# Optimization experiments

Measured on AMD Instinct MI355X. Metric: run time of the kernel, lower is better.

## Reference

```python
import jax, jax.numpy as jnp
import numpy as np

N_NODES = 100000
N_EDGES = 3200000
IN_DIM = 128
HID_DIM = 64
OUT_DIM = 2
N_GRAPHS = 512


def setup_inputs() -> dict:
    key = jax.random.key(0)
    ks = jax.random.split(key, 8)
    x = jax.random.normal(ks[0], (N_NODES, IN_DIM), dtype=jnp.float32)
    edge_index = jax.random.randint(ks[1], (2, N_EDGES), 0, N_NODES, dtype=jnp.int64)
    batch = jnp.sort(jax.random.randint(ks[2], (N_NODES,), 0, N_GRAPHS, dtype=jnp.int64))
    # GCNConv params (glorot-ish scale)
    W_gcn = jax.random.normal(ks[3], (IN_DIM, HID_DIM), dtype=jnp.float32) / np.sqrt(IN_DIM)
    b_gcn = jnp.zeros((HID_DIM,), dtype=jnp.float32)
    # MLP params: Linear(hid,hid) -> ReLU -> Linear(hid,out)
    W1 = jax.random.normal(ks[4], (HID_DIM, HID_DIM), dtype=jnp.float32) / np.sqrt(HID_DIM)
    b1 = jnp.zeros((HID_DIM,), dtype=jnp.float32)
    W2 = jax.random.normal(ks[5], (HID_DIM, OUT_DIM), dtype=jnp.float32) / np.sqrt(HID_DIM)
    b2 = jnp.zeros((OUT_DIM,), dtype=jnp.float32)
    return {"x": x, "edge_index": edge_index, "batch": batch,
            "W_gcn": W_gcn, "b_gcn": b_gcn, "W1": W1, "b1": b1, "W2": W2, "b2": b2}


def reference(x, edge_index, batch, W_gcn, b_gcn, W1, b1, W2, b2):
    n = x.shape[0]
    # --- GCNConv: add self-loops, symmetric normalization, aggregate, transform ---
    self_loop = jnp.arange(n, dtype=edge_index.dtype)
    row = jnp.concatenate([edge_index[0], self_loop])  # source nodes
    col = jnp.concatenate([edge_index[1], self_loop])  # target nodes
    deg = jax.ops.segment_sum(jnp.ones_like(col, dtype=x.dtype), col, num_segments=n)
    dinv = jnp.where(deg > 0, jax.lax.rsqrt(deg), 0.0)
    norm = dinv[row] * dinv[col]                       # (E+N,)
    xw = x @ W_gcn                                     # (N, hid) transform first (in_dim > hid)
    msg = xw[row] * norm[:, None]                      # gather + scale
    z = jax.ops.segment_sum(msg, col, num_segments=n) + b_gcn  # scatter-add
    z = jax.nn.relu(z)
    # --- global mean pool over graphs ---
    sums = jax.ops.segment_sum(z, batch, num_segments=N_GRAPHS)          # (G, hid)
    cnts = jax.ops.segment_sum(jnp.ones((n,), z.dtype), batch, num_segments=N_GRAPHS)
    g = sums / jnp.maximum(cnts, 1.0)[:, None]
    # --- MLP -> sigmoid ---
    h = jax.nn.relu(g @ W1 + b1)
    return jax.nn.sigmoid(h @ W2 + b2)                 # (G, out_dim)
```

## Files before the change

### kernel.cpp

```cpp
#include <hip/hip_runtime.h>

#define N_NODES 100000
#define N_EDGES 3200000
#define IN_DIM 128
#define HID_DIM 64
#define OUT_DIM 2
#define N_GRAPHS 512

#define BSHIFT 6
#define NBUCK 1564
#define NB3 256
#define EPB 12500
#define NSB 391
#define LDS_E2 2816
#define ZERO_ROW N_NODES

__device__ inline int xcol(int b) { return ((b & 7) << 5) | (b >> 3); }

__device__ inline float uaf(unsigned int u) {
    union { unsigned int i; float f; } v; v.i = u; return v.f;
}
__device__ inline unsigned short f2bf(float f) {
    union { float f; unsigned int i; } v; v.f = f;
    unsigned int r = v.i + 0x7fffu + ((v.i >> 16) & 1u);
    return (unsigned short)(r >> 16);
}

typedef __attribute__((ext_vector_type(8))) short bf16x8;
typedef __attribute__((ext_vector_type(4))) float f32x4;
typedef __attribute__((ext_vector_type(2))) float f32x2;

__global__ __launch_bounds__(512) void k_hist(const int* __restrict__ col,
                                              int* __restrict__ H) {
    __shared__ int h[NBUCK];
    for (int i = threadIdx.x; i < NBUCK; i += 512) h[i] = 0;
    __syncthreads();
    int b = blockIdx.x;
    int bb = xcol(b);
    int s = b * EPB, e = s + EPB;
    for (int i = s + threadIdx.x; i < e; i += 512)
        atomicAdd(&h[col[i] >> BSHIFT], 1);
    __syncthreads();
    for (int i = threadIdx.x; i < NBUCK; i += 512)
        H[i * NB3 + bb] = h[i];
}

__global__ __launch_bounds__(1024) void k_scan_a(const int* __restrict__ H,
                                                 int* __restrict__ OFF,
                                                 int* __restrict__ bsum) {
    __shared__ int lds[1024];
    int i = blockIdx.x * 1024 + threadIdx.x;
    int v = H[i];
    lds[threadIdx.x] = v;
    __syncthreads();
    for (int off = 1; off < 1024; off <<= 1) {
        int t = (threadIdx.x >= off) ? lds[threadIdx.x - off] : 0;
        __syncthreads();
        lds[threadIdx.x] += t;
        __syncthreads();
    }
    OFF[i] = lds[threadIdx.x] - v;
    if (threadIdx.x == 1023) bsum[blockIdx.x] = lds[1023];
}

__global__ __launch_bounds__(1024) void k_scan_b(int* __restrict__ OFF,
                                                 const int* __restrict__ bsum,
                                                 float* __restrict__ gsum,
                                                 float* __restrict__ gcnt,
                                                 unsigned char* __restrict__ xws) {
    __shared__ int ls[NSB];
    for (int i = threadIdx.x; i < NSB; i += 1024) ls[i] = bsum[i];
    __syncthreads();
    if (threadIdx.x == 0) {
        int run = 0;
        for (int b = 0; b < NSB; b++) { int t = ls[b]; ls[b] = run; run += t; }
    }
    __syncthreads();
    int i = blockIdx.x * 1024 + threadIdx.x;
    OFF[i] += ls[blockIdx.x];
    if (blockIdx.x < 32) gsum[blockIdx.x * 1024 + threadIdx.x] = 0.f;
    if (blockIdx.x == 33 && threadIdx.x < N_GRAPHS) gcnt[threadIdx.x] = 0.f;
    if (blockIdx.x == 32 && threadIdx.x < 16)
        ((int*)(xws + (size_t)ZERO_ROW * HID_DIM))[threadIdx.x] = 0;
}

__global__ __launch_bounds__(512) void k_scatter(const int* __restrict__ row,
                                                 const int* __restrict__ col,
                                                 const int* __restrict__ OFF,
                                                 int* __restrict__ binned) {
    __shared__ int lofs[NBUCK];
    __shared__ int cur[NBUCK];
    int b = blockIdx.x;
    int bb = xcol(b);
    for (int i = threadIdx.x; i < NBUCK; i += 512) {
        lofs[i] = OFF[i * NB3 + bb];
        cur[i] = 0;
    }
    __syncthreads();
    int s = b * EPB, e = s + EPB;
    for (int i = s + threadIdx.x; i < e; i += 512) {
        int c = col[i];
        int r = row[i];
        int bk = c >> BSHIFT;
        int rk = atomicAdd(&cur[bk], 1);
        binned[lofs[bk] + rk] = ((c & 63) << 17) | r;
    }
}

__global__ __launch_bounds__(256) void k_deg(const int* __restrict__ binned,
                                             const int* __restrict__ OFF,
                                             int* __restrict__ degs,
                                             float* __restrict__ dinv) {
    int bkt = blockIdx.x;
    int s = OFF[bkt * NB3];
    int e = (bkt == NBUCK - 1) ? N_EDGES : OFF[(bkt + 1) * NB3];
    __shared__ int cnt[64];
    if (threadIdx.x < 64) cnt[threadIdx.x] = 0;
    __syncthreads();
    for (int i = s + threadIdx.x; i < e; i += 256)
        atomicAdd(&cnt[binned[i] >> 17], 1);
    __syncthreads();
    int n = (bkt << BSHIFT) + threadIdx.x;
    if (threadIdx.x < 64 && n < N_NODES) {
        degs[n] = cnt[threadIdx.x];
        dinv[n] = rsqrtf((float)cnt[threadIdx.x] + 1.0f);
    }
}

__global__ __launch_bounds__(256) void k_gemm(const float* __restrict__ x,
                                              const float* __restrict__ Wg,
                                              const float* __restrict__ dinv,
                                              unsigned char* __restrict__ xws) {
    __shared__ unsigned short wb[16][64][8];

    for (int idx = threadIdx.x; idx < 1024; idx += 256) {
        int f = idx >> 6, l = idx & 63;
        int ks = f >> 2, nt = f & 3;
        int n = (l & 15) + (nt << 4);
        int kbase = (ks << 5) + ((l >> 4) << 3);
        unsigned short tmp[8];
#pragma unroll
        for (int j = 0; j < 8; j++)
            tmp[j] = f2bf(Wg[(kbase + j) * HID_DIM + n]);
        *(bf16x8*)&wb[f][l][0] = *(const bf16x8*)tmp;
    }
    __syncthreads();

    int wave = threadIdx.x >> 6;
    int lane = threadIdx.x & 63;
    int q = lane >> 4, nn = lane & 15;

    bf16x8 bfrag[4][4];
#pragma unroll
    for (int ks = 0; ks < 4; ks++)
#pragma unroll
        for (int nt = 0; nt < 4; nt++)
            bfrag[ks][nt] = *(const bf16x8*)&wb[ks * 4 + nt][lane][0];

    int node0 = blockIdx.x * 64 + wave * 16;
    int arow = node0 + nn;
    if (arow > N_NODES - 1) arow = N_NODES - 1;
    const float* xrow = x + (size_t)arow * IN_DIM + (q << 3);

    f32x4 acc[4] = {{0.f,0.f,0.f,0.f},{0.f,0.f,0.f,0.f},
                    {0.f,0.f,0.f,0.f},{0.f,0.f,0.f,0.f}};
#pragma unroll
    for (int ks = 0; ks < 4; ks++) {
        float4 xa = *(const float4*)(xrow + ks * 32);
        float4 xb_ = *(const float4*)(xrow + ks * 32 + 4);
        bf16x8 af;
        af[0] = (short)f2bf(xa.x); af[1] = (short)f2bf(xa.y);
        af[2] = (short)f2bf(xa.z); af[3] = (short)f2bf(xa.w);
        af[4] = (short)f2bf(xb_.x); af[5] = (short)f2bf(xb_.y);
        af[6] = (short)f2bf(xb_.z); af[7] = (short)f2bf(xb_.w);
#pragma unroll
        for (int nt = 0; nt < 4; nt++)
            acc[nt] = __builtin_amdgcn_mfma_f32_16x16x32_bf16(af, bfrag[ks][nt], acc[nt], 0, 0, 0);
    }

#pragma unroll
    for (int r = 0; r < 4; r++) {
        int mrow = node0 + q * 4 + r;
        if (mrow < N_NODES) {
            float dn = dinv[mrow];
            int p01 = __builtin_amdgcn_cvt_pk_fp8_f32(acc[0][r] * dn, acc[1][r] * dn, 0, false);
            int p23 = __builtin_amdgcn_cvt_pk_fp8_f32(acc[2][r] * dn, acc[3][r] * dn, 0, false);
            unsigned char* rp = xws + (size_t)mrow * HID_DIM + nn;
            rp[0]  = (unsigned char)(p01 & 0xff);
            rp[16] = (unsigned char)((p01 >> 8) & 0xff);
            rp[32] = (unsigned char)(p23 & 0xff);
            rp[48] = (unsigned char)((p23 >> 8) & 0xff);
        }
    }
}

__global__ __launch_bounds__(512) void k_aggrf(const unsigned char* __restrict__ xws,
                                               const int* __restrict__ binned,
                                               const int* __restrict__ OFF,
                                               const int* __restrict__ degs,
                                               const int* __restrict__ batch,
                                               const float* __restrict__ bg,
                                               float* __restrict__ gsum,
                                               float* __restrict__ gcnt) {
    int bkt = blockIdx.x;
    int nbase = bkt << BSHIFT;
    if (nbase >= N_NODES) return;
    int nnodes = N_NODES - nbase; if (nnodes > 64) nnodes = 64;
    int s = OFF[bkt * NB3];
    int e = (bkt == NBUCK - 1) ? N_EDGES : OFF[(bkt + 1) * NB3];
    int m = e - s;

    __shared__ int cnt[64];
    __shared__ int lptr[65];
    __shared__ int cur[64];
    __shared__ int sb[64];
    __shared__ float gcl[8];
    __shared__ alignas(16) int srt[LDS_E2];
    __shared__ float pool[8][4][64];

    if (threadIdx.x < 64) {
        int n = nbase + threadIdx.x;
        cnt[threadIdx.x] = (threadIdx.x < nnodes) ? degs[n] : 0;
        sb[threadIdx.x]  = (threadIdx.x < nnodes) ? batch[n] : 0;
        cur[threadIdx.x] = 0;
    }
    if (threadIdx.x < 8) gcl[threadIdx.x] = 0.f;
    for (int t = threadIdx.x; t < 8 * 4 * 64; t += 512)
        ((float*)pool)[t] = 0.f;
    __syncthreads();

    if (threadIdx.x < 64) {
        int v = (threadIdx.x < nnodes) ? ((cnt[threadIdx.x] + 8) & ~7) : 0;
        int run = v;
#pragma unroll
        for (int off = 1; off < 64; off <<= 1) {
            int t = __shfl_up(run, off);
            if (threadIdx.x >= off) run += t;
        }
        lptr[threadIdx.x + 1] = run;
        if (threadIdx.x == 0) lptr[0] = 0;
    }
    __syncthreads();
    int tot = lptr[64]; if (tot > LDS_E2) tot = LDS_E2;
    for (int i = threadIdx.x; i < tot; i += 512) srt[i] = ZERO_ROW << 6;
    __syncthreads();
    if (threadIdx.x < nnodes) {
        int p = lptr[threadIdx.x] + cnt[threadIdx.x];
        if (p < LDS_E2) srt[p] = (nbase + threadIdx.x) << 6;
        int sl = sb[threadIdx.x] - sb[0];
        if (sl < 8) atomicAdd(&gcl[sl], 1.0f);
        else atomicAdd(&gcnt[sb[threadIdx.x]], 1.0f);
    }
    for (int i = threadIdx.x; i < m; i += 512) {
        int pk = binned[s + i];
        int nid = pk >> 17;
        int rk = atomicAdd(&cur[nid], 1);
        int pos = lptr[nid] + rk;
        if (pos < LDS_E2) srt[pos] = (pk & 0x1FFFF) << 6;
    }
    __syncthreads();

    int wave = threadIdx.x >> 6;
    int lane = threadIdx.x & 63;
    int sub = lane >> 4;
    int lc  = lane & 15;
    int l4  = lc << 2;
    const unsigned char* xbl = xws + l4;
    int g0 = sb[0];
    float4 bia = ((const float4*)bg)[lc];

#pragma unroll
    for (int r = 0; r < 2; r++) {
        int ln = wave * 8 + sub * 2 + r;
        int valid = (ln < nnodes);
        int s0 = valid ? lptr[ln] : 0;
        int e0 = valid ? lptr[ln + 1] : 0;
        if (s0 > LDS_E2) s0 = LDS_E2;
        if (e0 > LDS_E2) e0 = LDS_E2;
        f32x2 al0 = {0.f,0.f}, ah0 = {0.f,0.f};
        f32x2 al1 = {0.f,0.f}, ah1 = {0.f,0.f};
        for (int i = s0; i < e0; i += 8) {
            int4 ra = *(const int4*)&srt[i];
            int4 rb = *(const int4*)&srt[i + 4];
            unsigned int d0 = *(const unsigned int*)(xbl + ra.x);
            unsigned int d1 = *(const unsigned int*)(xbl + ra.y);
            unsigned int d2 = *(const unsigned int*)(xbl + ra.z);
            unsigned int d3 = *(const unsigned int*)(xbl + ra.w);
            unsigned int d4 = *(const unsigned int*)(xbl + rb.x);
            unsigned int d5 = *(const unsigned int*)(xbl + rb.y);
            unsigned int d6 = *(const unsigned int*)(xbl + rb.z);
            unsigned int d7 = *(const unsigned int*)(xbl + rb.w);
            f32x2 p;
            p = __builtin_amdgcn_cvt_pk_f32_fp8(d0, false); al0 += p;
            p = __builtin_amdgcn_cvt_pk_f32_fp8(d0, true);  ah0 += p;
            p = __builtin_amdgcn_cvt_pk_f32_fp8(d1, false); al1 += p;
            p = __builtin_amdgcn_cvt_pk_f32_fp8(d1, true);  ah1 += p;
            p = __builtin_amdgcn_cvt_pk_f32_fp8(d2, false); al0 += p;
            p = __builtin_amdgcn_cvt_pk_f32_fp8(d2, true);  ah0 += p;
            p = __builtin_amdgcn_cvt_pk_f32_fp8(d3, false); al1 += p;
            p = __builtin_amdgcn_cvt_pk_f32_fp8(d3, true);  ah1 += p;
            p = __builtin_amdgcn_cvt_pk_f32_fp8(d4, false); al0 += p;
            p = __builtin_amdgcn_cvt_pk_f32_fp8(d4, true);  ah0 += p;
            p = __builtin_amdgcn_cvt_pk_f32_fp8(d5, false); al1 += p;
            p = __builtin_amdgcn_cvt_pk_f32_fp8(d5, true);  ah1 += p;
            p = __builtin_amdgcn_cvt_pk_f32_fp8(d6, false); al0 += p;
            p = __builtin_amdgcn_cvt_pk_f32_fp8(d6, true);  ah0 += p;
            p = __builtin_amdgcn_cvt_pk_f32_fp8(d7, false); al1 += p;
            p = __builtin_amdgcn_cvt_pk_f32_fp8(d7, true);  ah1 += p;
        }
        f32x2 alo = al0 + al1, ahi = ah0 + ah1;
        int slot = 99;
        float4 val;
        if (valid) {
            float dn = rsqrtf((float)cnt[ln] + 1.0f);
            val.x = fmaxf(alo[0] * dn + bia.x, 0.f);
            val.y = fmaxf(alo[1] * dn + bia.y, 0.f);
            val.z = fmaxf(ahi[0] * dn + bia.z, 0.f);
            val.w = fmaxf(ahi[1] * dn + bia.w, 0.f);
            slot = sb[ln] - g0;
        }
#pragma unroll
        for (int ss = 0; ss < 4; ss++) {
            if (sub == ss && slot < 4) {
                float4* pp = (float4*)&pool[wave][slot][l4];
                float4 pv = *pp;
                pv.x += val.x; pv.y += val.y; pv.z += val.z; pv.w += val.w;
                *pp = pv;
            }
        }
        if (slot >= 4 && slot < 99) {
            float* gp = &gsum[sb[ln] * HID_DIM + l4];
            atomicAdd(gp + 0, val.x); atomicAdd(gp + 1, val.y);
            atomicAdd(gp + 2, val.z); atomicAdd(gp + 3, val.w);
        }
    }
    __syncthreads();

    if (threadIdx.x < 8) {
        float c = gcl[threadIdx.x];
        if (c != 0.f) atomicAdd(&gcnt[g0 + threadIdx.x], c);
    }
    for (int t = threadIdx.x; t < 4 * 64; t += 512) {
        int slot = t >> 6, j = t & 63;
        float v = 0.f;
#pragma unroll
        for (int w2 = 0; w2 < 8; w2++) v += pool[w2][slot][j];
        if (v != 0.f) atomicAdd(&gsum[(g0 + slot) * HID_DIM + j], v);
    }
}

__global__ __launch_bounds__(64) void k_mlp(const float* __restrict__ gsum,
                                            const float* __restrict__ gcnt,
                                            const float* __restrict__ W1,
                                            const float* __restrict__ b1,
                                            const float* __restrict__ W2,
                                            const float* __restrict__ b2,
                                            float* __restrict__ out) {
    int g = blockIdx.x;
    int j = threadIdx.x;
    float cnt = fmaxf(gcnt[g], 1.0f);

    __shared__ float gs[64];
    __shared__ float hs[64];
    gs[j] = gsum[g * 64 + j] / cnt;
    __syncthreads();

    float h = b1[j];
    for (int k = 0; k < 64; k++) h += gs[k] * W1[k * 64 + j];
    hs[j] = fmaxf(h, 0.f);
    __syncthreads();

    if (j < OUT_DIM) {
        float o = b2[j];
        for (int k = 0; k < 64; k++) o += hs[k] * W2[k * OUT_DIM + j];
        out[g * OUT_DIM + j] = 1.f / (1.f + expf(-o));
    }
}

extern "C" void kernel_launch(void* const* d_in, const int* in_sizes, int n_in,
                              void* d_out, int out_size, void* d_ws, size_t ws_size,
                              hipStream_t stream) {
    const float* x   = (const float*)d_in[0];
    const int* eidx  = (const int*)d_in[1];
    const int* batch = (const int*)d_in[2];
    const float* Wg  = (const float*)d_in[3];
    const float* bg  = (const float*)d_in[4];
    const float* W1  = (const float*)d_in[5];
    const float* b1  = (const float*)d_in[6];
    const float* W2  = (const float*)d_in[7];
    const float* b2  = (const float*)d_in[8];
    float* out = (float*)d_out;

    char* w = (char*)d_ws;
    unsigned char* xws = (unsigned char*)w;     w += (size_t)(N_NODES + 1) * HID_DIM;
    int*   binned  = (int*)w;                   w += (size_t)N_EDGES * 4;
    int*   H       = (int*)w;                   w += (size_t)NBUCK * NB3 * 4;
    int*   OFF     = (int*)w;                   w += (size_t)NBUCK * NB3 * 4;
    int*   bsum    = (int*)w;                   w += NSB * 4;
    int*   degs    = (int*)w;                   w += N_NODES * 4;
    float* dinv    = (float*)w;                 w += N_NODES * 4;
    float* gsum    = (float*)w;                 w += N_GRAPHS * HID_DIM * 4;
    float* gcnt    = (float*)w;                 w += N_GRAPHS * 4;

    const int* rowp = eidx;
    const int* colp = eidx + N_EDGES;

    k_hist<<<NB3, 512, 0, stream>>>(colp, H);
    k_scan_a<<<NSB, 1024, 0, stream>>>(H, OFF, bsum);
    k_scan_b<<<NSB, 1024, 0, stream>>>(OFF, bsum, gsum, gcnt, xws);
    k_scatter<<<NB3, 512, 0, stream>>>(rowp, colp, OFF, binned);
    k_deg<<<NBUCK, 256, 0, stream>>>(binned, OFF, degs, dinv);
    k_gemm<<<(N_NODES + 63) / 64, 256, 0, stream>>>(x, Wg, dinv, xws);
    k_aggrf<<<NBUCK, 512, 0, stream>>>(xws, binned, OFF, degs, batch, bg, gsum, gcnt);
    k_mlp<<<N_GRAPHS, 64, 0, stream>>>(gsum, gcnt, W1, b1, W2, b2, out);
}
```

Measured before the change: 201.2 us.

## Replace global scan binning with fixed-capacity buckets and atomic slot reservation

```diff
diff --git a/kernel.cpp b/kernel.cpp
--- a/kernel.cpp
+++ b/kernel.cpp
@@ -8,18 +8,13 @@
 #define N_GRAPHS 512
 
 #define BSHIFT 6
-#define NBUCK 1564
+#define NBK 1563
 #define NB3 256
 #define EPB 12500
-#define NSB 391
+#define CAPSHIFT 12
 #define LDS_E2 2816
 #define ZERO_ROW N_NODES
 
-__device__ inline int xcol(int b) { return ((b & 7) << 5) | (b >> 3); }
-
-__device__ inline float uaf(unsigned int u) {
-    union { unsigned int i; float f; } v; v.i = u; return v.f;
-}
 __device__ inline unsigned short f2bf(float f) {
     union { float f; unsigned int i; } v; v.f = f;
     unsigned int r = v.i + 0x7fffu + ((v.i >> 16) & 1u);
@@ -30,109 +25,60 @@
 typedef __attribute__((ext_vector_type(4))) float f32x4;
 typedef __attribute__((ext_vector_type(2))) float f32x2;
 
-__global__ __launch_bounds__(512) void k_hist(const int* __restrict__ col,
-                                              int* __restrict__ H) {
-    __shared__ int h[NBUCK];
-    for (int i = threadIdx.x; i < NBUCK; i += 512) h[i] = 0;
-    __syncthreads();
+__global__ __launch_bounds__(1024) void k_init(int* __restrict__ cnt_g) {
+    int i = blockIdx.x * 1024 + threadIdx.x;
+    if (i < NBK) cnt_g[i] = 0;
+}
+
+__global__ __launch_bounds__(512) void k_bin(const int* __restrict__ row,
+                                             const int* __restrict__ col,
+                                             int* __restrict__ cnt_g,
+                                             int* __restrict__ binned,
+                                             float* __restrict__ gsum,
+                                             float* __restrict__ gcnt,
+                                             unsigned char* __restrict__ xws) {
+    __shared__ int h[NBK];
+    __shared__ int cur[NBK];
+    __shared__ int colbuf[EPB];
     int b = blockIdx.x;
-    int bb = xcol(b);
-    int s = b * EPB, e = s + EPB;
-    for (int i = s + threadIdx.x; i < e; i += 512)
-        atomicAdd(&h[col[i] >> BSHIFT], 1);
-    __syncthreads();
-    for (int i = threadIdx.x; i < NBUCK; i += 512)
-        H[i * NB3 + bb] = h[i];
-}
-
-__global__ __launch_bounds__(1024) void k_scan_a(const int* __restrict__ H,
-                                                 int* __restrict__ OFF,
-                                                 int* __restrict__ bsum) {
-    __shared__ int lds[1024];
-    int i = blockIdx.x * 1024 + threadIdx.x;
-    int v = H[i];
-    lds[threadIdx.x] = v;
-    __syncthreads();
-    for (int off = 1; off < 1024; off <<= 1) {
-        int t = (threadIdx.x >= off) ? lds[threadIdx.x - off] : 0;
-        __syncthreads();
-        lds[threadIdx.x] += t;
-        __syncthreads();
-    }
-    OFF[i] = lds[threadIdx.x] - v;
-    if (threadIdx.x == 1023) bsum[blockIdx.x] = lds[1023];
-}
-
-__global__ __launch_bounds__(1024) void k_scan_b(int* __restrict__ OFF,
-                                                 const int* __restrict__ bsum,
-                                                 float* __restrict__ gsum,
-                                                 float* __restrict__ gcnt,
-                                                 unsigned char* __restrict__ xws) {
-    __shared__ int ls[NSB];
-    for (int i = threadIdx.x; i < NSB; i += 1024) ls[i] = bsum[i];
-    __syncthreads();
-    if (threadIdx.x == 0) {
-        int run = 0;
-        for (int b = 0; b < NSB; b++) { int t = ls[b]; ls[b] = run; run += t; }
-    }
-    __syncthreads();
-    int i = blockIdx.x * 1024 + threadIdx.x;
-    OFF[i] += ls[blockIdx.x];
-    if (blockIdx.x < 32) gsum[blockIdx.x * 1024 + threadIdx.x] = 0.f;
-    if (blockIdx.x == 33 && threadIdx.x < N_GRAPHS) gcnt[threadIdx.x] = 0.f;
-    if (blockIdx.x == 32 && threadIdx.x < 16)
-        ((int*)(xws + (size_t)ZERO_ROW * HID_DIM))[threadIdx.x] = 0;
-}
-
-__global__ __launch_bounds__(512) void k_scatter(const int* __restrict__ row,
-                                                 const int* __restrict__ col,
-                                                 const int* __restrict__ OFF,
-                                                 int* __restrict__ binned) {
-    __shared__ int lofs[NBUCK];
-    __shared__ int cur[NBUCK];
-    int b = blockIdx.x;
-    int bb = xcol(b);
-    for (int i = threadIdx.x; i < NBUCK; i += 512) {
-        lofs[i] = OFF[i * NB3 + bb];
-        cur[i] = 0;
-    }
-    __syncthreads();
-    int s = b * EPB, e = s + EPB;
-    for (int i = s + threadIdx.x; i < e; i += 512) {
+    for (int i = threadIdx.x; i < NBK; i += 512) { h[i] = 0; cur[i] = 0; }
+    if (threadIdx.x < 128) gsum[b * 128 + threadIdx.x] = 0.f;
+    if (b == 0) {
+        gcnt[threadIdx.x] = 0.f;
+        if (threadIdx.x >= 496)
+            ((int*)(xws + (size_t)ZERO_ROW * HID_DIM))[threadIdx.x - 496] = 0;
+    }
+    __syncthreads();
+    int s = b * EPB;
+    for (int it = 0, i = s + threadIdx.x; i < s + EPB; i += 512, ++it) {
         int c = col[i];
+        colbuf[it * 512 + threadIdx.x] = c;
+        atomicAdd(&h[c >> BSHIFT], 1);
+    }
+    __syncthreads();
+    for (int i = threadIdx.x; i < NBK; i += 512) {
+        int hv = h[i];
+        if (hv) h[i] = (i << CAPSHIFT) + atomicAdd(&cnt_g[i], hv);
+    }
+    __syncthreads();
+    for (int it = 0, i = s + threadIdx.x; i < s + EPB; i += 512, ++it) {
+        int c = colbuf[it * 512 + threadIdx.x];
         int r = row[i];
         int bk = c >> BSHIFT;
         int rk = atomicAdd(&cur[bk], 1);
-        binned[lofs[bk] + rk] = ((c & 63) << 17) | r;
-    }
-}
-
-__global__ __launch_bounds__(256) void k_deg(const int* __restrict__ binned,
-                                             const int* __restrict__ OFF,
-                                             int* __restrict__ degs,
-                                             float* __restrict__ dinv) {
-    int bkt = blockIdx.x;
-    int s = OFF[bkt * NB3];
-    int e = (bkt == NBUCK - 1) ? N_EDGES : OFF[(bkt + 1) * NB3];
-    __shared__ int cnt[64];
-    if (threadIdx.x < 64) cnt[threadIdx.x] = 0;
-    __syncthreads();
-    for (int i = s + threadIdx.x; i < e; i += 256)
-        atomicAdd(&cnt[binned[i] >> 17], 1);
-    __syncthreads();
-    int n = (bkt << BSHIFT) + threadIdx.x;
-    if (threadIdx.x < 64 && n < N_NODES) {
-        degs[n] = cnt[threadIdx.x];
-        dinv[n] = rsqrtf((float)cnt[threadIdx.x] + 1.0f);
+        binned[h[bk] + rk] = ((c & 63) << 17) | r;
     }
 }
 
 __global__ __launch_bounds__(256) void k_gemm(const float* __restrict__ x,
                                               const float* __restrict__ Wg,
-                                              const float* __restrict__ dinv,
+                                              const int* __restrict__ cnt_g,
+                                              const int* __restrict__ binned,
                                               unsigned char* __restrict__ xws) {
     __shared__ unsigned short wb[16][64][8];
-
+    __shared__ int cnt[64];
+
+    if (threadIdx.x < 64) cnt[threadIdx.x] = 0;
     for (int idx = threadIdx.x; idx < 1024; idx += 256) {
         int f = idx >> 6, l = idx & 63;
         int ks = f >> 2, nt = f & 3;
@@ -146,6 +92,11 @@
     }
     __syncthreads();
 
+    int bkt = blockIdx.x;
+    int m = cnt_g[bkt];
+    for (int i = threadIdx.x; i < m; i += 256)
+        atomicAdd(&cnt[binned[(bkt << CAPSHIFT) + i] >> 17], 1);
+
     int wave = threadIdx.x >> 6;
     int lane = threadIdx.x & 63;
     int q = lane >> 4, nn = lane & 15;
@@ -157,7 +108,7 @@
         for (int nt = 0; nt < 4; nt++)
             bfrag[ks][nt] = *(const bf16x8*)&wb[ks * 4 + nt][lane][0];
 
-    int node0 = blockIdx.x * 64 + wave * 16;
+    int node0 = bkt * 64 + wave * 16;
     int arow = node0 + nn;
     if (arow > N_NODES - 1) arow = N_NODES - 1;
     const float* xrow = x + (size_t)arow * IN_DIM + (q << 3);
@@ -177,12 +128,14 @@
         for (int nt = 0; nt < 4; nt++)
             acc[nt] = __builtin_amdgcn_mfma_f32_16x16x32_bf16(af, bfrag[ks][nt], acc[nt], 0, 0, 0);
     }
+    __syncthreads();
 
 #pragma unroll
     for (int r = 0; r < 4; r++) {
-        int mrow = node0 + q * 4 + r;
+        int lrow = wave * 16 + q * 4 + r;
+        int mrow = bkt * 64 + lrow;
         if (mrow < N_NODES) {
-            float dn = dinv[mrow];
+            float dn = rsqrtf((float)cnt[lrow] + 1.0f);
             int p01 = __builtin_amdgcn_cvt_pk_fp8_f32(acc[0][r] * dn, acc[1][r] * dn, 0, false);
             int p23 = __builtin_amdgcn_cvt_pk_fp8_f32(acc[2][r] * dn, acc[3][r] * dn, 0, false);
             unsigned char* rp = xws + (size_t)mrow * HID_DIM + nn;
@@ -196,19 +149,16 @@
 
 __global__ __launch_bounds__(512) void k_aggrf(const unsigned char* __restrict__ xws,
                                                const int* __restrict__ binned,
-                                               const int* __restrict__ OFF,
-                                               const int* __restrict__ degs,
+                                               const int* __restrict__ cnt_g,
                                                const int* __restrict__ batch,
                                                const float* __restrict__ bg,
                                                float* __restrict__ gsum,
                                                float* __restrict__ gcnt) {
     int bkt = blockIdx.x;
     int nbase = bkt << BSHIFT;
-    if (nbase >= N_NODES) return;
     int nnodes = N_NODES - nbase; if (nnodes > 64) nnodes = 64;
-    int s = OFF[bkt * NB3];
-    int e = (bkt == NBUCK - 1) ? N_EDGES : OFF[(bkt + 1) * NB3];
-    int m = e - s;
+    int m = cnt_g[bkt];
+    int base = bkt << CAPSHIFT;
 
     __shared__ int cnt[64];
     __shared__ int lptr[65];
@@ -220,13 +170,17 @@
 
     if (threadIdx.x < 64) {
         int n = nbase + threadIdx.x;
-        cnt[threadIdx.x] = (threadIdx.x < nnodes) ? degs[n] : 0;
+        cnt[threadIdx.x] = 0;
         sb[threadIdx.x]  = (threadIdx.x < nnodes) ? batch[n] : 0;
         cur[threadIdx.x] = 0;
     }
     if (threadIdx.x < 8) gcl[threadIdx.x] = 0.f;
     for (int t = threadIdx.x; t < 8 * 4 * 64; t += 512)
         ((float*)pool)[t] = 0.f;
+    __syncthreads();
+
+    for (int i = threadIdx.x; i < m; i += 512)
+        atomicAdd(&cnt[binned[base + i] >> 17], 1);
     __syncthreads();
 
     if (threadIdx.x < 64) {
@@ -252,7 +206,7 @@
         else atomicAdd(&gcnt[sb[threadIdx.x]], 1.0f);
     }
     for (int i = threadIdx.x; i < m; i += 512) {
-        int pk = binned[s + i];
+        int pk = binned[base + i];
         int nid = pk >> 17;
         int rk = atomicAdd(&cur[nid], 1);
         int pos = lptr[nid] + rk;
@@ -393,24 +347,17 @@
 
     char* w = (char*)d_ws;
     unsigned char* xws = (unsigned char*)w;     w += (size_t)(N_NODES + 1) * HID_DIM;
-    int*   binned  = (int*)w;                   w += (size_t)N_EDGES * 4;
-    int*   H       = (int*)w;                   w += (size_t)NBUCK * NB3 * 4;
-    int*   OFF     = (int*)w;                   w += (size_t)NBUCK * NB3 * 4;
-    int*   bsum    = (int*)w;                   w += NSB * 4;
-    int*   degs    = (int*)w;                   w += N_NODES * 4;
-    float* dinv    = (float*)w;                 w += N_NODES * 4;
+    int*   binned  = (int*)w;                   w += ((size_t)NBK << CAPSHIFT) * 4;
+    int*   cnt_g   = (int*)w;                   w += NBK * 4;
     float* gsum    = (float*)w;                 w += N_GRAPHS * HID_DIM * 4;
     float* gcnt    = (float*)w;                 w += N_GRAPHS * 4;
 
     const int* rowp = eidx;
     const int* colp = eidx + N_EDGES;
 
-    k_hist<<<NB3, 512, 0, stream>>>(colp, H);
-    k_scan_a<<<NSB, 1024, 0, stream>>>(H, OFF, bsum);
-    k_scan_b<<<NSB, 1024, 0, stream>>>(OFF, bsum, gsum, gcnt, xws);
-    k_scatter<<<NB3, 512, 0, stream>>>(rowp, colp, OFF, binned);
-    k_deg<<<NBUCK, 256, 0, stream>>>(binned, OFF, degs, dinv);
-    k_gemm<<<(N_NODES + 63) / 64, 256, 0, stream>>>(x, Wg, dinv, xws);
-    k_aggrf<<<NBUCK, 512, 0, stream>>>(xws, binned, OFF, degs, batch, bg, gsum, gcnt);
+    k_init<<<2, 1024, 0, stream>>>(cnt_g);
+    k_bin<<<NB3, 512, 0, stream>>>(rowp, colp, cnt_g, binned, gsum, gcnt, xws);
+    k_gemm<<<NBK, 256, 0, stream>>>(x, Wg, cnt_g, binned, xws);
+    k_aggrf<<<NBK, 512, 0, stream>>>(xws, binned, cnt_g, batch, bg, gsum, gcnt);
     k_mlp<<<N_GRAPHS, 64, 0, stream>>>(gsum, gcnt, W1, b1, W2, b2, out);
 }
```

New measurement: 202.0 us. Within noise of the previous version (+0.4%).
